# Kernel optimization log

Measured on AMD Instinct MI355X. Metric: run time of the kernel, lower is better.

The kernel has to match this reference:

```python
import jax, jax.numpy as jnp
import numpy as np

B, T = 1024, 320
EEG_CH, GEO_CH, F1, HID, OUT = 64, 18, 8, 32, 4
THETA0, BETA, TAU_A = 0.5, 1.8, 0.36
EPS = 1e-5


def _bn(x, s, b, m, v):
    # eval-mode BatchNorm with running stats (flax default eps 1e-5)
    return (x - m) * jax.lax.rsqrt(v + EPS) * s + b


def _dwconv(x, w, b, groups):
    # depthwise temporal conv, x: (B, T, C), w: (K, 1, C*F1), SAME padding
    y = jax.lax.conv_general_dilated(x, w, (1,), 'SAME', dimension_numbers=('NWC', 'WIO', 'NWC'), feature_group_count=groups)
    return y + b


def _spike(x):
    return jnp.where(x >= 0.0, 1.0, 0.0)


def _forward(x_eeg, x_geo, eeg_conv_w, eeg_conv_b, eeg_bn1_s, eeg_bn1_b, eeg_bn1_m, eeg_bn1_v, eeg_dense_w, eeg_dense_b, eeg_bn2_s, eeg_bn2_b, eeg_bn2_m, eeg_bn2_v, geo_conv_w, geo_conv_b, geo_bn1_s, geo_bn1_b, geo_bn1_m, geo_bn1_v, geo_dense_w, geo_dense_b, geo_bn2_s, geo_bn2_b, geo_bn2_m, geo_bn2_v, gamma, fc1_w, fc1_b, fc2_w, fc2_b):
    Bc = x_eeg.shape[0]
    xe = _bn(_dwconv(x_eeg, eeg_conv_w, eeg_conv_b, EEG_CH), eeg_bn1_s, eeg_bn1_b, eeg_bn1_m, eeg_bn1_v)
    xe = _bn(xe @ eeg_dense_w + eeg_dense_b, eeg_bn2_s, eeg_bn2_b, eeg_bn2_m, eeg_bn2_v)
    eeg_enc = jax.nn.relu(xe)                      # (B, T, HID)
    xg = _bn(_dwconv(x_geo, geo_conv_w, geo_conv_b, GEO_CH), geo_bn1_s, geo_bn1_b, geo_bn1_m, geo_bn1_v)
    xg = _bn(xg @ geo_dense_w + geo_dense_b, geo_bn2_s, geo_bn2_b, geo_bn2_m, geo_bn2_v)
    geo_mod = jax.nn.sigmoid(xg)                   # (B, T, HID)

    def step(carry, inp):
        m1, m2, m3, ma, eta, mli, prev = carry
        ce, cg = inp
        m1 = 0.9 * m1 + ce; s1 = _spike(m1 - 0.7); m1 = m1 * (1.0 - s1)
        m2 = 0.8 * m2 + ce; s2 = _spike(m2 - 0.5); m2 = m2 * (1.0 - s2)
        m3 = 0.6 * m3 + ce; s3 = _spike(m3 - 0.3); m3 = m3 * (1.0 - s3)
        hr = (s1 + s2 + s3) / 3.0
        eta = TAU_A * eta + (1.0 - TAU_A) * prev
        theta = THETA0 + BETA * eta - gamma * cg
        ma = 0.8 * ma + hr
        sa = _spike(ma - theta)
        ma = ma * (1.0 - sa)
        mli = 0.9 * mli + sa
        return (m1, m2, m3, ma, eta, mli, sa), mli

    z = jnp.zeros((Bc, HID), x_eeg.dtype)
    _, seq = jax.lax.scan(step, (z, z, z, z, z, z, z), (jnp.swapaxes(eeg_enc, 0, 1), jnp.swapaxes(geo_mod, 0, 1)))
    seq = jnp.transpose(seq, (1, 2, 0))            # (B, HID, T)
    win = seq.reshape(Bc, HID, 10, 32)
    dp = (jnp.mean(win[..., 16:], -1) - jnp.mean(win[..., :16], -1)).reshape(Bc, HID * 10)
    return jax.nn.elu(dp @ fc1_w + fc1_b) @ fc2_w + fc2_b


def setup_inputs() -> dict:
    ks = iter(jax.random.split(jax.random.key(0), 48))
    def rn(shape, s=1.0):
        return jax.random.normal(next(ks), shape, jnp.float32) * s
    ECH, GCH = EEG_CH * F1, GEO_CH * F1
    return {
        'x_eeg': rn((B, T, EEG_CH)),
        'x_geo': rn((B, T, GEO_CH)),
        'eeg_conv_w': rn((32, 1, ECH), 0.05), 'eeg_conv_b': jnp.zeros((ECH,), jnp.float32),
        'eeg_bn1_s': 1.0 + rn((ECH,), 0.1), 'eeg_bn1_b': rn((ECH,), 0.1),
        'eeg_bn1_m': rn((ECH,), 0.1), 'eeg_bn1_v': 1.0 + 0.1 * jax.random.uniform(next(ks), (ECH,), jnp.float32),
        'eeg_dense_w': rn((ECH, HID), 0.05), 'eeg_dense_b': jnp.zeros((HID,), jnp.float32),
        'eeg_bn2_s': 1.0 + rn((HID,), 0.1), 'eeg_bn2_b': rn((HID,), 0.1),
        'eeg_bn2_m': rn((HID,), 0.1), 'eeg_bn2_v': 1.0 + 0.1 * jax.random.uniform(next(ks), (HID,), jnp.float32),
        'geo_conv_w': rn((32, 1, GCH), 0.05), 'geo_conv_b': jnp.zeros((GCH,), jnp.float32),
        'geo_bn1_s': 1.0 + rn((GCH,), 0.1), 'geo_bn1_b': rn((GCH,), 0.1),
        'geo_bn1_m': rn((GCH,), 0.1), 'geo_bn1_v': 1.0 + 0.1 * jax.random.uniform(next(ks), (GCH,), jnp.float32),
        'geo_dense_w': rn((GCH, HID), 0.05), 'geo_dense_b': jnp.zeros((HID,), jnp.float32),
        'geo_bn2_s': 1.0 + rn((HID,), 0.1), 'geo_bn2_b': rn((HID,), 0.1),
        'geo_bn2_m': rn((HID,), 0.1), 'geo_bn2_v': 1.0 + 0.1 * jax.random.uniform(next(ks), (HID,), jnp.float32),
        'gamma': jnp.full((HID,), 0.5, jnp.float32),
        'fc1_w': rn((HID * 10, 128), 0.05), 'fc1_b': jnp.zeros((128,), jnp.float32),
        'fc2_w': rn((128, OUT), 0.05), 'fc2_b': jnp.zeros((OUT,), jnp.float32),
    }


def reference(x_eeg, x_geo, eeg_conv_w, eeg_conv_b, eeg_bn1_s, eeg_bn1_b, eeg_bn1_m, eeg_bn1_v, eeg_dense_w, eeg_dense_b, eeg_bn2_s, eeg_bn2_b, eeg_bn2_m, eeg_bn2_v, geo_conv_w, geo_conv_b, geo_bn1_s, geo_bn1_b, geo_bn1_m, geo_bn1_v, geo_dense_w, geo_dense_b, geo_bn2_s, geo_bn2_b, geo_bn2_m, geo_bn2_v, gamma, fc1_w, fc1_b, fc2_w, fc2_b):
    return _forward(x_eeg, x_geo, eeg_conv_w, eeg_conv_b, eeg_bn1_s, eeg_bn1_b, eeg_bn1_m, eeg_bn1_v, eeg_dense_w, eeg_dense_b, eeg_bn2_s, eeg_bn2_b, eeg_bn2_m, eeg_bn2_v, geo_conv_w, geo_conv_b, geo_bn1_s, geo_bn1_b, geo_bn1_m, geo_bn1_v, geo_dense_w, geo_dense_b, geo_bn2_s, geo_bn2_b, geo_bn2_m, geo_bn2_v, gamma, fc1_w, fc1_b, fc2_w, fc2_b)
```

## Files before the change

kernel.cpp:

```cpp
#include <hip/hip_runtime.h>
#include <hip/hip_bf16.h>
#include <math.h>

#define BSZ   1024
#define TLEN  320
#define EEGC  64
#define GEOC  18
#define ECH   512
#define GCH   144
#define HID   32
#define KW    32
#define TT    32
#define NT    (TLEN/TT)

#define OFF_ENC  0
#define OFF_MOD  (OFF_ENC + BSZ*TLEN*HID)
#define OFF_DP   (OFF_MOD + BSZ*TLEN*HID)
#define OFF_CWE  (OFF_DP + BSZ*HID*10)
#define OFF_CWG  (OFF_CWE + ECH*KW)
#define OFF_DWE  (OFF_CWG + GCH*KW)
#define OFF_DWG  (OFF_DWE + ECH*HID)
#define OFF_BTE  (OFF_DWG + GCH*HID)
#define OFF_BTG  (OFF_BTE + HID)
#define OFF_GAM  (OFF_BTG + HID)

struct P29 { const float* p[29]; };

__global__ __launch_bounds__(256) void prep_kernel(P29 P, float* __restrict__ ws)
{
    const int tid = threadIdx.x;
    float* convW_e = ws + OFF_CWE;
    float* convW_g = ws + OFF_CWG;
    float* dW_e    = ws + OFF_DWE;
    float* dW_g    = ws + OFF_DWG;

    for (int i = tid; i < ECH * KW; i += 256) {
        int c = i >> 5, k = i & 31;
        float A1 = P.p[2][c] * rsqrtf(P.p[5][c] + 1e-5f);
        convW_e[c * KW + k] = P.p[0][(size_t)k * ECH + c] * A1;
    }
    for (int i = tid; i < GCH * KW; i += 256) {
        int c = i >> 5, k = i & 31;
        float A1 = P.p[14][c] * rsqrtf(P.p[17][c] + 1e-5f);
        convW_g[c * KW + k] = P.p[12][(size_t)k * GCH + c] * A1;
    }
    for (int i = tid; i < ECH * HID; i += 256) {
        int h = i & 31;
        float A2 = P.p[8][h] * rsqrtf(P.p[11][h] + 1e-5f);
        dW_e[i] = P.p[6][i] * A2;
    }
    for (int i = tid; i < GCH * HID; i += 256) {
        int h = i & 31;
        float A2 = P.p[20][h] * rsqrtf(P.p[23][h] + 1e-5f);
        dW_g[i] = P.p[18][i] * A2;
    }
    for (int i = tid; i < HID; i += 256) ws[OFF_GAM + i] = P.p[24][i];

    if (tid < HID) {
        int h = tid;
        float A2 = P.p[8][h] * rsqrtf(P.p[11][h] + 1e-5f);
        float s = 0.f;
        for (int c = 0; c < ECH; ++c) {
            float A1 = P.p[2][c] * rsqrtf(P.p[5][c] + 1e-5f);
            float C1 = (P.p[1][c] - P.p[4][c]) * A1 + P.p[3][c];
            s += C1 * P.p[6][(size_t)c * HID + h];
        }
        ws[OFF_BTE + h] = A2 * (s + P.p[7][h] - P.p[10][h]) + P.p[9][h];
    } else if (tid >= 64 && tid < 64 + HID) {
        int h = tid - 64;
        float A2 = P.p[20][h] * rsqrtf(P.p[23][h] + 1e-5f);
        float s = 0.f;
        for (int c = 0; c < GCH; ++c) {
            float A1 = P.p[14][c] * rsqrtf(P.p[17][c] + 1e-5f);
            float C1 = (P.p[13][c] - P.p[16][c]) * A1 + P.p[15][c];
            s += C1 * P.p[18][(size_t)c * HID + h];
        }
        ws[OFF_BTG + h] = A2 * (s + P.p[19][h] - P.p[22][h]) + P.p[21][h];
    }
}

__device__ __forceinline__ void conv_stream(const float4* __restrict__ xp4,
                                            const float* __restrict__ w,
                                            float* __restrict__ acc)
{
    float4 cur = xp4[0];
    #pragma unroll
    for (int j4 = 0; j4 < 12; ++j4) {
        float4 nxt = (j4 < 11) ? xp4[j4 + 1] : cur;
        #pragma unroll
        for (int i2 = 0; i2 < 4; ++i2) {
            const int i = j4 * 4 + i2;
            const float xv = (i2 == 0) ? cur.x : (i2 == 1) ? cur.y
                           : (i2 == 2) ? cur.z : cur.w;
            const int tlo = (i - 31 > 0) ? (i - 31) : 0;
            const int thi = (i < 15) ? i : 15;
            #pragma unroll
            for (int t = tlo; t <= thi; ++t)
                acc[t] = fmaf(xv, w[i - t], acc[t]);
        }
        cur = nxt;
    }
}

__global__ __launch_bounds__(256, 4)
void path_eeg(const float* __restrict__ x, float* __restrict__ ws)
{
    __shared__ __align__(16) float xsT[16 * 68];
    __shared__ __align__(16) float czs[128 * 36];

    const int b   = blockIdx.y;
    const int t0  = blockIdx.x * TT;
    const int tid = threadIdx.x;
    const float* convW = ws + OFF_CWE;
    const float* dW    = ws + OFF_DWE;
    float* enc         = ws + OFF_ENC;
    float* cz          = czs;

    const float* xb = x + (size_t)b * (TLEN * EEGC);

    const int tg = tid & 7, hg = (tid >> 3) & 7, q = tid >> 6;
    const int c_loc = tid & 127, th = tid >> 7;
    float a00=0,a01=0,a02=0,a03=0, a10=0,a11=0,a12=0,a13=0;
    float a20=0,a21=0,a22=0,a23=0, a30=0,a31=0,a32=0,a33=0;

    #pragma unroll 1
    for (int ph = 0; ph < 4; ++ph) {
        if (ph) __syncthreads();
        if (tid < 252) {
            const int sj = tid >> 2, sc4 = tid & 3;
            const int st = t0 - 15 + sj;
            float4 sv = make_float4(0.f, 0.f, 0.f, 0.f);
            if (st >= 0 && st < TLEN)
                sv = *(const float4*)(xb + (size_t)st * EEGC + ph * 16 + sc4 * 4);
            float* p = &xsT[(sc4 * 4) * 68 + sj];
            p[0] = sv.x; p[68] = sv.y; p[136] = sv.z; p[204] = sv.w;
        }
        __syncthreads();
        {
            const int c   = ph * 128 + c_loc;
            const int chl = c_loc >> 3;
            float w[KW];
            const float4* wp4 = (const float4*)(convW + c * KW);
            #pragma unroll
            for (int k4 = 0; k4 < 8; ++k4) {
                float4 v = wp4[k4];
                w[4*k4+0]=v.x; w[4*k4+1]=v.y; w[4*k4+2]=v.z; w[4*k4+3]=v.w;
            }
            float acc[16];
            #pragma unroll
            for (int t = 0; t < 16; ++t) acc[t] = 0.f;
            conv_stream((const float4*)(&xsT[chl * 68 + th * 16]), w, acc);
            float4* czp = (float4*)(cz + c_loc * 36 + th * 16);
            czp[0] = make_float4(acc[0],  acc[1],  acc[2],  acc[3]);
            czp[1] = make_float4(acc[4],  acc[5],  acc[6],  acc[7]);
            czp[2] = make_float4(acc[8],  acc[9],  acc[10], acc[11]);
            czp[3] = make_float4(acc[12], acc[13], acc[14], acc[15]);
        }
        __syncthreads();
        {
            const float* dWh = dW + (size_t)(ph * 128 + q * 32) * HID + hg * 4;
            const float* czb = cz + (q * 32) * 36 + tg * 4;
            float4 wvb[4], cvb[2];
            wvb[0] = *(const float4*)(dWh + 0 * HID);
            wvb[1] = *(const float4*)(dWh + 1 * HID);
            wvb[2] = *(const float4*)(dWh + 2 * HID);
            wvb[3] = *(const float4*)(dWh + 3 * HID);
            cvb[0] = *(const float4*)(czb + 0 * 36);
            cvb[1] = *(const float4*)(czb + 1 * 36);
            #pragma unroll
            for (int ci = 0; ci < 32; ++ci) {
                float4 cv = cvb[ci & 1];
                float4 wv = wvb[ci & 3];
                if (ci + 2 < 32) cvb[ci & 1] = *(const float4*)(czb + (ci + 2) * 36);
                if (ci + 4 < 32) wvb[ci & 3] = *(const float4*)(dWh + (ci + 4) * HID);
                a00 = fmaf(cv.x, wv.x, a00); a01 = fmaf(cv.x, wv.y, a01);
                a02 = fmaf(cv.x, wv.z, a02); a03 = fmaf(cv.x, wv.w, a03);
                a10 = fmaf(cv.y, wv.x, a10); a11 = fmaf(cv.y, wv.y, a11);
                a12 = fmaf(cv.y, wv.z, a12); a13 = fmaf(cv.y, wv.w, a13);
                a20 = fmaf(cv.z, wv.x, a20); a21 = fmaf(cv.z, wv.y, a21);
                a22 = fmaf(cv.z, wv.z, a22); a23 = fmaf(cv.z, wv.w, a23);
                a30 = fmaf(cv.w, wv.x, a30); a31 = fmaf(cv.w, wv.y, a31);
                a32 = fmaf(cv.w, wv.z, a32); a33 = fmaf(cv.w, wv.w, a33);
            }
        }
    }

    __syncthreads();
    float* stash = czs;
    {
        const int s = (tid >> 1) & 3;
        float4* sp = (float4*)(stash + tid * 16);
        sp[s ^ 0] = make_float4(a00,a01,a02,a03);
        sp[s ^ 1] = make_float4(a10,a11,a12,a13);
        sp[s ^ 2] = make_float4(a20,a21,a22,a23);
        sp[s ^ 3] = make_float4(a30,a31,a32,a33);
    }
    __syncthreads();
    {
        const int t = tid >> 3, hq = tid & 7;
        const int pg = (t & 3) ^ (t >> 3);
        float4 v = make_float4(0.f,0.f,0.f,0.f);
        #pragma unroll
        for (int qq = 0; qq < 4; ++qq) {
            const int partner = qq * 64 + hq * 8 + (t >> 2);
            float4 s = *(const float4*)(stash + partner * 16 + pg * 4);
            v.x += s.x; v.y += s.y; v.z += s.z; v.w += s.w;
        }
        float4 bias = *(const float4*)(ws + OFF_BTE + hq * 4);
        v.x = fmaxf(v.x + bias.x, 0.f);
        v.y = fmaxf(v.y + bias.y, 0.f);
        v.z = fmaxf(v.z + bias.z, 0.f);
        v.w = fmaxf(v.w + bias.w, 0.f);
        *(float4*)(enc + ((size_t)(b * TLEN + t0 + t)) * HID + hq * 4) = v;
    }
}

__device__ __forceinline__ void geo_conv_unit(const float* __restrict__ convW,
                                              const float* __restrict__ xsT,
                                              float* __restrict__ cz,
                                              int c, int th)
{
    float w[KW];
    const float4* wp4 = (const float4*)(convW + c * KW);
    #pragma unroll
    for (int k4 = 0; k4 < 8; ++k4) {
        float4 v = wp4[k4];
        w[4*k4+0]=v.x; w[4*k4+1]=v.y; w[4*k4+2]=v.z; w[4*k4+3]=v.w;
    }
    float acc[16];
    #pragma unroll
    for (int t = 0; t < 16; ++t) acc[t] = 0.f;
    conv_stream((const float4*)(xsT + (c >> 3) * 68 + th * 16), w, acc);
    float4* czp = (float4*)(cz + c * 36 + th * 16);
    czp[0] = make_float4(acc[0],  acc[1],  acc[2],  acc[3]);
    czp[1] = make_float4(acc[4],  acc[5],  acc[6],  acc[7]);
    czp[2] = make_float4(acc[8],  acc[9],  acc[10], acc[11]);
    czp[3] = make_float4(acc[12], acc[13], acc[14], acc[15]);
}

__global__ __launch_bounds__(256, 4) void path_geo(const float* __restrict__ x,
                                                   float* __restrict__ ws)
{
    __shared__ __align__(16) float xsT[GEOC * 68];
    __shared__ __align__(16) float cz[GCH * 36];

    const int b   = blockIdx.y;
    const int t0  = blockIdx.x * TT;
    const int tid = threadIdx.x;
    const float* convW = ws + OFF_CWG;
    const float* dW    = ws + OFF_DWG;
    float* mod         = ws + OFF_MOD;

    const float* xb = x + (size_t)b * (TLEN * GEOC);
    for (int i = tid; i < 63 * GEOC; i += 256) {
        int j = i / GEOC, ch = i - j * GEOC;
        int t = t0 - 15 + j;
        xsT[ch * 68 + j] = (t >= 0 && t < TLEN) ? xb[(size_t)t * GEOC + ch] : 0.f;
    }
    __syncthreads();

    geo_conv_unit(convW, xsT, cz, tid >> 1, tid & 1);
    if (tid < 32)
        geo_conv_unit(convW, xsT, cz, 128 + (tid >> 1), tid & 1);
    __syncthreads();

    const int tg = tid & 7, hg = (tid >> 3) & 7, q = tid >> 6;
    float a00=0,a01=0,a02=0,a03=0, a10=0,a11=0,a12=0,a13=0;
    float a20=0,a21=0,a22=0,a23=0, a30=0,a31=0,a32=0,a33=0;
    {
        const float* dWh = dW + (size_t)(q * 36) * HID + hg * 4;
        const float* czb = cz + (q * 36) * 36 + tg * 4;
        #pragma unroll 2
        for (int ci = 0; ci < 36; ++ci) {
            float4 cv = *(const float4*)(czb + ci * 36);
            float4 wv = *(const float4*)(dWh + ci * HID);
            a00 = fmaf(cv.x, wv.x, a00); a01 = fmaf(cv.x, wv.y, a01);
            a02 = fmaf(cv.x, wv.z, a02); a03 = fmaf(cv.x, wv.w, a03);
            a10 = fmaf(cv.y, wv.x, a10); a11 = fmaf(cv.y, wv.y, a11);
            a12 = fmaf(cv.y, wv.z, a12); a13 = fmaf(cv.y, wv.w, a13);
            a20 = fmaf(cv.z, wv.x, a20); a21 = fmaf(cv.z, wv.y, a21);
            a22 = fmaf(cv.z, wv.z, a22); a23 = fmaf(cv.z, wv.w, a23);
            a30 = fmaf(cv.w, wv.x, a30); a31 = fmaf(cv.w, wv.y, a31);
            a32 = fmaf(cv.w, wv.z, a32); a33 = fmaf(cv.w, wv.w, a33);
        }
    }
    __syncthreads();
    float* stash = cz;
    {
        float4* sp = (float4*)(stash + tid * 20);
        sp[0] = make_float4(a00,a01,a02,a03);
        sp[1] = make_float4(a10,a11,a12,a13);
        sp[2] = make_float4(a20,a21,a22,a23);
        sp[3] = make_float4(a30,a31,a32,a33);
    }
    __syncthreads();
    {
        const int t = tid >> 3, hq = tid & 7;
        float4 v = make_float4(0.f,0.f,0.f,0.f);
        #pragma unroll
        for (int qq = 0; qq < 4; ++qq) {
            const int partner = qq * 64 + hq * 8 + (t >> 2);
            float4 s = *(const float4*)(stash + partner * 20 + (t & 3) * 4);
            v.x += s.x; v.y += s.y; v.z += s.z; v.w += s.w;
        }
        float4 bias = *(const float4*)(ws + OFF_BTG + hq * 4);
        v.x = 1.f / (1.f + expf(-(v.x + bias.x)));
        v.y = 1.f / (1.f + expf(-(v.y + bias.y)));
        v.z = 1.f / (1.f + expf(-(v.z + bias.z)));
        v.w = 1.f / (1.f + expf(-(v.w + bias.w)));
        *(float4*)(mod + ((size_t)(b * TLEN + t0 + t)) * HID + hq * 4) = v;
    }
}

__global__ __launch_bounds__(128) void scan_kernel(float* __restrict__ ws)
{
    const int idx = blockIdx.x * 128 + threadIdx.x;
    const int b = idx >> 5, h = idx & 31;
    const float g = ws[OFF_GAM + h];
    const float* pe = ws + OFF_ENC + (size_t)b * TLEN * HID + h;
    const float* pg = ws + OFF_MOD + (size_t)b * TLEN * HID + h;
    float m1 = 0.f, m2 = 0.f, m3 = 0.f, ma = 0.f, eta = 0.f, mli = 0.f, prev = 0.f;
    float acc_lo = 0.f, acc_hi = 0.f;
    float* dpp = ws + OFF_DP + b * (HID * 10) + h * 10;
    int w = 0;
    #pragma unroll 8
    for (int t = 0; t < TLEN; ++t) {
        const float ce = pe[t * HID];
        const float cg = pg[t * HID];
        m1 = 0.9f * m1 + ce; float s1 = ((m1 - 0.7f) >= 0.f) ? 1.f : 0.f; m1 = m1 * (1.f - s1);
        m2 = 0.8f * m2 + ce; float s2 = ((m2 - 0.5f) >= 0.f) ? 1.f : 0.f; m2 = m2 * (1.f - s2);
        m3 = 0.6f * m3 + ce; float s3 = ((m3 - 0.3f) >= 0.f) ? 1.f : 0.f; m3 = m3 * (1.f - s3);
        const float hr = (s1 + s2 + s3) / 3.0f;
        eta = 0.36f * eta + 0.64f * prev;
        const float theta = 0.5f + 1.8f * eta - g * cg;
        ma = 0.8f * ma + hr;
        const float sa = ((ma - theta) >= 0.f) ? 1.f : 0.f;
        ma = ma * (1.f - sa);
        mli = 0.9f * mli + sa;
        prev = sa;
        if ((t & 31) < 16) acc_lo += mli; else acc_hi += mli;
        if ((t & 31) == 31) {
            dpp[w] = acc_hi * (1.f / 16.f) - acc_lo * (1.f / 16.f);
            acc_lo = 0.f; acc_hi = 0.f; ++w;
        }
    }
}

__global__ __launch_bounds__(128) void head_kernel(
    const float* __restrict__ ws,
    const float* __restrict__ f1w, const float* __restrict__ f1b,
    const float* __restrict__ f2w, const float* __restrict__ f2b,
    float* __restrict__ out)
{
    __shared__ float act[128];
    const int b = blockIdx.x, j = threadIdx.x;
    const float* dpb = ws + OFF_DP + b * 320;
    float a = f1b[j];
    for (int i = 0; i < 320; ++i)
        a = fmaf(dpb[i], f1w[i * 128 + j], a);
    act[j] = (a > 0.f) ? a : expm1f(a);
    __syncthreads();
    if (j < 4) {
        float o = f2b[j];
        for (int jj = 0; jj < 128; ++jj)
            o = fmaf(act[jj], f2w[jj * 4 + j], o);
        out[b * 4 + j] = o;
    }
}

extern "C" void kernel_launch(void* const* d_in, const int* in_sizes, int n_in,
                              void* d_out, int out_size, void* d_ws, size_t ws_size,
                              hipStream_t stream)
{
    float* ws = (float*)d_ws;

    P29 P;
    for (int k = 0; k < 29; ++k) P.p[k] = (const float*)d_in[k + 2];
    prep_kernel<<<1, 256, 0, stream>>>(P, ws);

    path_eeg<<<dim3(NT, BSZ), 256, 0, stream>>>((const float*)d_in[0], ws);
    path_geo<<<dim3(NT, BSZ), 256, 0, stream>>>((const float*)d_in[1], ws);

    scan_kernel<<<(BSZ * HID) / 128, 128, 0, stream>>>(ws);

    head_kernel<<<BSZ, 128, 0, stream>>>(
        ws, (const float*)d_in[27], (const float*)d_in[28],
        (const float*)d_in[29], (const float*)d_in[30], (float*)d_out);
}
```

Baseline: 840.6 us.

## Double-buffer scan inputs, parallelize prep bias reduction, split head accumulators

The scan kernel now loads its inputs in 16-step chunks into register arrays, prefetching the next chunk while the current one is processed, which removes per-step global-load latency from the serial recurrence. The prep kernel spreads the folded-bias reductions across all 256 threads and combines partial sums through shared memory instead of using 32 threads per branch. The head kernel uses four independent FMA accumulators to break the dependency chain. The register arrays increase register pressure, and the changed summation order alters floating-point rounding slightly.

```diff
diff --git a/kernel.cpp b/kernel.cpp
--- a/kernel.cpp
+++ b/kernel.cpp
@@ -28,6 +28,8 @@
 
 __global__ __launch_bounds__(256) void prep_kernel(P29 P, float* __restrict__ ws)
 {
+    __shared__ float pse[8][32];
+    __shared__ float psg[8][32];
     const int tid = threadIdx.x;
     float* convW_e = ws + OFF_CWE;
     float* convW_g = ws + OFF_CWG;
@@ -56,25 +58,35 @@
     }
     for (int i = tid; i < HID; i += 256) ws[OFF_GAM + i] = P.p[24][i];
 
+    {
+        const int h = tid & 31, part = tid >> 5;
+        float s = 0.f;
+        for (int c = part * 64; c < part * 64 + 64; ++c) {
+            float A1 = P.p[2][c] * rsqrtf(P.p[5][c] + 1e-5f);
+            float C1 = (P.p[1][c] - P.p[4][c]) * A1 + P.p[3][c];
+            s += C1 * P.p[6][(size_t)c * HID + h];
+        }
+        pse[part][h] = s;
+        float sg = 0.f;
+        for (int c = part * 18; c < part * 18 + 18; ++c) {
+            float A1 = P.p[14][c] * rsqrtf(P.p[17][c] + 1e-5f);
+            float C1 = (P.p[13][c] - P.p[16][c]) * A1 + P.p[15][c];
+            sg += C1 * P.p[18][(size_t)c * HID + h];
+        }
+        psg[part][h] = sg;
+    }
+    __syncthreads();
     if (tid < HID) {
         int h = tid;
         float A2 = P.p[8][h] * rsqrtf(P.p[11][h] + 1e-5f);
-        float s = 0.f;
-        for (int c = 0; c < ECH; ++c) {
-            float A1 = P.p[2][c] * rsqrtf(P.p[5][c] + 1e-5f);
-            float C1 = (P.p[1][c] - P.p[4][c]) * A1 + P.p[3][c];
-            s += C1 * P.p[6][(size_t)c * HID + h];
-        }
+        float s = pse[0][h] + pse[1][h] + pse[2][h] + pse[3][h]
+                + pse[4][h] + pse[5][h] + pse[6][h] + pse[7][h];
         ws[OFF_BTE + h] = A2 * (s + P.p[7][h] - P.p[10][h]) + P.p[9][h];
     } else if (tid >= 64 && tid < 64 + HID) {
         int h = tid - 64;
         float A2 = P.p[20][h] * rsqrtf(P.p[23][h] + 1e-5f);
-        float s = 0.f;
-        for (int c = 0; c < GCH; ++c) {
-            float A1 = P.p[14][c] * rsqrtf(P.p[17][c] + 1e-5f);
-            float C1 = (P.p[13][c] - P.p[16][c]) * A1 + P.p[15][c];
-            s += C1 * P.p[18][(size_t)c * HID + h];
-        }
+        float s = psg[0][h] + psg[1][h] + psg[2][h] + psg[3][h]
+                + psg[4][h] + psg[5][h] + psg[6][h] + psg[7][h];
         ws[OFF_BTG + h] = A2 * (s + P.p[19][h] - P.p[22][h]) + P.p[21][h];
     }
 }
@@ -312,6 +324,20 @@
     }
 }
 
+#define SSTEP(CE, CG) { \
+    const float ce = (CE), cg = (CG); \
+    m1 = 0.9f * m1 + ce; float s1 = ((m1 - 0.7f) >= 0.f) ? 1.f : 0.f; m1 = m1 * (1.f - s1); \
+    m2 = 0.8f * m2 + ce; float s2 = ((m2 - 0.5f) >= 0.f) ? 1.f : 0.f; m2 = m2 * (1.f - s2); \
+    m3 = 0.6f * m3 + ce; float s3 = ((m3 - 0.3f) >= 0.f) ? 1.f : 0.f; m3 = m3 * (1.f - s3); \
+    const float hr = (s1 + s2 + s3) / 3.0f; \
+    eta = 0.36f * eta + 0.64f * prev; \
+    const float theta = 0.5f + 1.8f * eta - g * cg; \
+    ma = 0.8f * ma + hr; \
+    const float sa = ((ma - theta) >= 0.f) ? 1.f : 0.f; \
+    ma = ma * (1.f - sa); \
+    mli = 0.9f * mli + sa; \
+    prev = sa; }
+
 __global__ __launch_bounds__(128) void scan_kernel(float* __restrict__ ws)
 {
     const int idx = blockIdx.x * 128 + threadIdx.x;
@@ -319,30 +345,44 @@
     const float g = ws[OFF_GAM + h];
     const float* pe = ws + OFF_ENC + (size_t)b * TLEN * HID + h;
     const float* pg = ws + OFF_MOD + (size_t)b * TLEN * HID + h;
+    float* dpp = ws + OFF_DP + b * (HID * 10) + h * 10;
+
     float m1 = 0.f, m2 = 0.f, m3 = 0.f, ma = 0.f, eta = 0.f, mli = 0.f, prev = 0.f;
     float acc_lo = 0.f, acc_hi = 0.f;
-    float* dpp = ws + OFF_DP + b * (HID * 10) + h * 10;
-    int w = 0;
-    #pragma unroll 8
-    for (int t = 0; t < TLEN; ++t) {
-        const float ce = pe[t * HID];
-        const float cg = pg[t * HID];
-        m1 = 0.9f * m1 + ce; float s1 = ((m1 - 0.7f) >= 0.f) ? 1.f : 0.f; m1 = m1 * (1.f - s1);
-        m2 = 0.8f * m2 + ce; float s2 = ((m2 - 0.5f) >= 0.f) ? 1.f : 0.f; m2 = m2 * (1.f - s2);
-        m3 = 0.6f * m3 + ce; float s3 = ((m3 - 0.3f) >= 0.f) ? 1.f : 0.f; m3 = m3 * (1.f - s3);
-        const float hr = (s1 + s2 + s3) / 3.0f;
-        eta = 0.36f * eta + 0.64f * prev;
-        const float theta = 0.5f + 1.8f * eta - g * cg;
-        ma = 0.8f * ma + hr;
-        const float sa = ((ma - theta) >= 0.f) ? 1.f : 0.f;
-        ma = ma * (1.f - sa);
-        mli = 0.9f * mli + sa;
-        prev = sa;
-        if ((t & 31) < 16) acc_lo += mli; else acc_hi += mli;
-        if ((t & 31) == 31) {
-            dpp[w] = acc_hi * (1.f / 16.f) - acc_lo * (1.f / 16.f);
-            acc_lo = 0.f; acc_hi = 0.f; ++w;
-        }
+
+    float ceA[16], cgA[16], ceB[16], cgB[16];
+
+    #pragma unroll
+    for (int i = 0; i < 16; ++i) { ceA[i] = pe[i * HID]; cgA[i] = pg[i * HID]; }
+
+    #pragma unroll 1
+    for (int ch = 0; ch < 20; ch += 2) {
+        const int baseB = (ch + 1) * 16;
+        #pragma unroll
+        for (int i = 0; i < 16; ++i) {
+            ceB[i] = pe[(baseB + i) * HID];
+            cgB[i] = pg[(baseB + i) * HID];
+        }
+        #pragma unroll
+        for (int i = 0; i < 16; ++i) {
+            SSTEP(ceA[i], cgA[i]);
+            acc_lo += mli;
+        }
+        if (ch + 2 < 20) {
+            const int baseA = (ch + 2) * 16;
+            #pragma unroll
+            for (int i = 0; i < 16; ++i) {
+                ceA[i] = pe[(baseA + i) * HID];
+                cgA[i] = pg[(baseA + i) * HID];
+            }
+        }
+        #pragma unroll
+        for (int i = 0; i < 16; ++i) {
+            SSTEP(ceB[i], cgB[i]);
+            acc_hi += mli;
+        }
+        dpp[ch >> 1] = acc_hi * (1.f / 16.f) - acc_lo * (1.f / 16.f);
+        acc_lo = 0.f; acc_hi = 0.f;
     }
 }
 
@@ -355,9 +395,15 @@
     __shared__ float act[128];
     const int b = blockIdx.x, j = threadIdx.x;
     const float* dpb = ws + OFF_DP + b * 320;
-    float a = f1b[j];
-    for (int i = 0; i < 320; ++i)
-        a = fmaf(dpb[i], f1w[i * 128 + j], a);
+    float a0 = 0.f, a1 = 0.f, a2 = 0.f, a3 = 0.f;
+    #pragma unroll 4
+    for (int i = 0; i < 320; i += 4) {
+        a0 = fmaf(dpb[i + 0], f1w[(i + 0) * 128 + j], a0);
+        a1 = fmaf(dpb[i + 1], f1w[(i + 1) * 128 + j], a1);
+        a2 = fmaf(dpb[i + 2], f1w[(i + 2) * 128 + j], a2);
+        a3 = fmaf(dpb[i + 3], f1w[(i + 3) * 128 + j], a3);
+    }
+    float a = f1b[j] + ((a0 + a1) + (a2 + a3));
     act[j] = (a > 0.f) ? a : expm1f(a);
     __syncthreads();
     if (j < 4) {
```

After: 686.4 us. 1.22x faster.
